# Kernel optimization log

Measured on AMD Instinct MI355X. Metric: run time of the kernel, lower is better.

Reference implementation:

```python
import jax, jax.numpy as jnp
import numpy as np

N_NODES = 100000

def gcn_conv(x, src, dst, dinv, W, b):
    # PyG GCNConv: out[i] = sum_{j->i} dinv[j]*dinv[i] * (x @ W)[j] + b
    h = x @ W                                   # [N, Cout]
    norm = (dinv[src] * dinv[dst])[:, None]     # [E, 1]
    msg = h[src] * norm                         # edge-wise gather + scale
    agg = jax.ops.segment_sum(msg, dst, num_segments=N_NODES)
    return agg + b

def setup_inputs() -> dict:
    key = jax.random.key(0)
    ks = jax.random.split(key, 8)
    x = jax.random.normal(ks[0], (N_NODES, 128), dtype=jnp.float32)
    edge_index = jax.random.randint(ks[1], (2, 1600000), 0, N_NODES, dtype=jnp.int64)
    s = 0.05
    W1 = jax.random.normal(ks[2], (128, 256), dtype=jnp.float32) * s
    b1 = jnp.zeros((256,), dtype=jnp.float32)
    W2 = jax.random.normal(ks[3], (256, 128), dtype=jnp.float32) * s
    b2 = jnp.zeros((128,), dtype=jnp.float32)
    W3 = jax.random.normal(ks[4], (128, 64), dtype=jnp.float32) * s
    b3 = jnp.zeros((64,), dtype=jnp.float32)
    return {"x": x, "edge_index": edge_index, "W1": W1, "b1": b1,
            "W2": W2, "b2": b2, "W3": W3, "b3": b3}

def reference(x, edge_index, W1, b1, W2, b2, W3, b3):
    # add self-loops once (same graph for all three convs)
    loops = jnp.arange(N_NODES, dtype=edge_index.dtype)
    src = jnp.concatenate([edge_index[0], loops])
    dst = jnp.concatenate([edge_index[1], loops])
    # symmetric degree normalization (deg computed on destination, with self-loops)
    deg = jax.ops.segment_sum(jnp.ones_like(dst, dtype=x.dtype), dst, num_segments=N_NODES)
    dinv = jnp.where(deg > 0, jax.lax.rsqrt(jnp.maximum(deg, 1.0)), 0.0)
    h = jax.nn.relu(gcn_conv(x, src, dst, dinv, W1, b1))   # dropout = identity (eval)
    h = jax.nn.relu(gcn_conv(h, src, dst, dinv, W2, b2))
    h = jax.nn.relu(gcn_conv(h, src, dst, dinv, W3, b3))
    return jax.nn.log_softmax(h, axis=1)
```

## Files before the change

### kernel.cpp

```cpp
#include <hip/hip_runtime.h>
#include <math.h>

#define N_NODES 100000
#define N_EDGES 1600000
#define CHUNK 4096
#define NBLK_P ((N_EDGES + CHUNK - 1) / CHUNK)
#define NPAD 100064
#define BSHIFT 8
#define NBUCK ((N_NODES + 255) / 256)
#define BCAP 6144

typedef __attribute__((ext_vector_type(8))) short bf16x8;
typedef __attribute__((ext_vector_type(4))) float f32x4;
typedef __attribute__((ext_vector_type(2))) float f32x2;

__device__ __forceinline__ unsigned short f2bf(float f) {
    unsigned int u = __builtin_bit_cast(unsigned int, f);
    u += 0x7fffu + ((u >> 16) & 1u);
    return (unsigned short)(u >> 16);
}
__device__ __forceinline__ unsigned char f2fp8(float f) {
    return (unsigned char)(__builtin_amdgcn_cvt_pk_fp8_f32(f, f, 0, false) & 0xff);
}
__device__ __forceinline__ f32x2 fp8x2f(unsigned short u) {
    return __builtin_amdgcn_cvt_pk_f32_fp8((int)u, false);
}
__device__ __forceinline__ float fp8f(unsigned char u) {
    return __builtin_amdgcn_cvt_f32_fp8((int)u, 0);
}


__global__ __launch_bounds__(1024) void edge_count_kernel(const int* __restrict__ dst,
                                                          int* __restrict__ bcnt) {
    __shared__ int lh[NBUCK];
    int tid = threadIdx.x;
    if (tid < NBUCK) lh[tid] = 0;
    __syncthreads();
    long base = (long)blockIdx.x * CHUNK;
#pragma unroll
    for (int p = 0; p < CHUNK; p += 1024) {
        long e = base + p + tid;
        if (e < N_EDGES) atomicAdd(&lh[dst[e] >> BSHIFT], 1);
    }
    __syncthreads();
    if (tid < NBUCK) bcnt[tid * NBLK_P + blockIdx.x] = lh[tid];
}


__global__ void bucket_scan_kernel(int* __restrict__ bcnt, int* __restrict__ btot) {
    int bu = blockIdx.x, lane = threadIdx.x;
    int base = 0;
    for (int i0 = 0; i0 < NBLK_P; i0 += 64) {
        int i = i0 + lane;
        int v = (i < NBLK_P) ? bcnt[bu * NBLK_P + i] : 0;
        int orig = v;
#pragma unroll
        for (int off = 1; off < 64; off <<= 1) {
            int t = __shfl_up(v, off);
            if (lane >= off) v += t;
        }
        if (i < NBLK_P) bcnt[bu * NBLK_P + i] = base + v - orig;
        base += __shfl(v, 63);
    }
    if (lane == 0) btot[bu] = base;
}

__global__ void bbase_scan_kernel(const int* __restrict__ btot, int* __restrict__ bbase) {
    __shared__ int tmp[512];
    int i = threadIdx.x;
    int v = (i < NBUCK) ? btot[i] : 0;
    tmp[i] = v;
    __syncthreads();
    for (int off = 1; off < 512; off <<= 1) {
        int t = (i >= off) ? tmp[i - off] : 0;
        __syncthreads();
        tmp[i] += t;
        __syncthreads();
    }
    if (i < NBUCK) bbase[i] = tmp[i] - v;
}


__global__ __launch_bounds__(1024) void part_scatter_kernel(
        const int* __restrict__ src, const int* __restrict__ dst,
        const int* __restrict__ bcnt, const int* __restrict__ bbase,
        int* __restrict__ part) {
    __shared__ int lh[NBUCK];
    int tid = threadIdx.x;
    if (tid < NBUCK) lh[tid] = 0;
    __syncthreads();
    long base = (long)blockIdx.x * CHUNK;
#pragma unroll
    for (int p = 0; p < CHUNK; p += 1024) {
        long e = base + p + tid;
        if (e < N_EDGES) {
            int s = src[e], d = dst[e];
            int bu = d >> BSHIFT;
            int lr = atomicAdd(&lh[bu], 1);
            int pos = bbase[bu] + bcnt[bu * NBLK_P + blockIdx.x] + lr;
            part[pos] = s | ((d & 255) << 17);
        }
    }
}


__global__ __launch_bounds__(512) void bucket_deg_kernel(
        const int* __restrict__ part, const int* __restrict__ bbase,
        const int* __restrict__ btot, int* __restrict__ rowp,
        float* __restrict__ dinv) {
    __shared__ int lcnt[256];
    __shared__ int lscan[256];
    int b = blockIdx.x;
    int node0 = b << BSHIFT;
    int start = bbase[b];
    int cnt = btot[b];
    int tid = threadIdx.x;
    if (tid < 256) lcnt[tid] = 0;
    __syncthreads();
    for (int e = tid; e < cnt; e += 512)
        atomicAdd(&lcnt[part[start + e] >> 17], 1);
    __syncthreads();
    int v = 0;
    if (tid < 256) { v = lcnt[tid]; lscan[tid] = v; }
    __syncthreads();
    for (int off = 1; off < 256; off <<= 1) {
        int t = (tid < 256 && tid >= off) ? lscan[tid - off] : 0;
        __syncthreads();
        if (tid < 256) lscan[tid] += t;
        __syncthreads();
    }
    if (tid < 256) {
        int n = node0 + tid;
        if (n < N_NODES) {
            rowp[n] = start + lscan[tid] - v;
            dinv[n] = rsqrtf(1.0f + (float)v);
        }
    }
    if (b == NBUCK - 1 && tid == 0) rowp[N_NODES] = N_EDGES;
}


__global__ __launch_bounds__(512) void final_scatter_lds_kernel(
        const int* __restrict__ part, const float* __restrict__ dinv,
        const int* __restrict__ rowp, const int* __restrict__ bbase,
        const int* __restrict__ btot, int2* __restrict__ sedge) {
    __shared__ int lcurs[256];
    __shared__ int2 buf[BCAP];
    int b = blockIdx.x;
    int node0 = b << BSHIFT;
    int start = bbase[b];
    int cnt = btot[b];
    int tid = threadIdx.x;
    if (tid < 256) {
        int n = node0 + tid;
        lcurs[tid] = (n < N_NODES) ? (rowp[n] - start) : cnt;
    }
    __syncthreads();
    for (int e = tid; e < cnt; e += 512) {
        int r = part[start + e];
        int s = r & 0x1FFFF;
        int lpos = atomicAdd(&lcurs[r >> 17], 1);
        int2 rec; rec.x = s; rec.y = __float_as_int(dinv[s]);
        if (lpos < BCAP) buf[lpos] = rec;
        else sedge[start + lpos] = rec;
    }
    __syncthreads();
    int lim = min(cnt, BCAP);
    for (int e = tid; e < lim; e += 512)
        sedge[start + e] = buf[e];
}


__global__ void cvt_x_kernel(const float* __restrict__ x, unsigned char* __restrict__ xb) {
    long i = (long)blockIdx.x * blockDim.x + threadIdx.x;
    if (i >= (long)N_NODES * 128 / 4) return;
    float4 v = ((const float4*)x)[i];
    int p0 = __builtin_amdgcn_cvt_pk_fp8_f32(v.x, v.y, 0, false);
    int p1 = __builtin_amdgcn_cvt_pk_fp8_f32(v.z, v.w, 0, false);
    ((unsigned int*)xb)[i] = ((unsigned int)p0 & 0xffffu) | ((unsigned int)p1 << 16);
}

__global__ void cvt_w_all_kernel(const float* __restrict__ W1, const float* __restrict__ W2,
                                 const float* __restrict__ W3,
                                 unsigned short* __restrict__ Wt1,
                                 unsigned short* __restrict__ Wt2,
                                 unsigned short* __restrict__ Wt3) {
    int i = blockIdx.x * blockDim.x + threadIdx.x;
    if (i < 32768) {
        int k = i >> 8, m = i & 255;
        Wt1[m * 128 + k] = f2bf(W1[i]);
    } else if (i < 65536) {
        int j = i - 32768;
        int k = j >> 7, m = j & 127;
        Wt2[m * 256 + k] = f2bf(W2[j]);
    } else if (i < 73728) {
        int j = i - 65536;
        int k = j >> 6, m = j & 63;
        Wt3[m * 128 + k] = f2bf(W3[j]);
    }
}


template<int C, bool BIAS, bool RELU, bool LOGSM, bool OUTF32>
__global__ __launch_bounds__(64) void agg_csr_kernel(
                               const unsigned char* __restrict__ h8,
                               const float* __restrict__ dinv,
                               const int* __restrict__ rowptr,
                               const int2* __restrict__ sedge,
                               const float* __restrict__ bias, void* __restrict__ outv) {
    constexpr int V = C / 64;
    int gw = blockIdx.x;
    int lane = threadIdx.x;
    if (gw >= N_NODES) return;

    float di = dinv[gw];
    int st = rowptr[gw];
    int cnt = rowptr[gw + 1] - st;
    float a0, a1 = 0.0f;
    if constexpr (V == 2) {
        unsigned short u = ((const unsigned short*)(h8 + (long)gw * C))[lane];
        f32x2 f = fp8x2f(u);
        a0 = di * f.x; a1 = di * f.y;
    } else {
        a0 = di * fp8f(h8[(long)gw * C + lane]);
    }

    int k = 0;
    for (; k + 8 <= cnt; k += 8) {
        int2 r[8];
#pragma unroll
        for (int j = 0; j < 8; ++j) r[j] = sedge[st + k + j];
        if constexpr (V == 2) {
            unsigned short u[8];
#pragma unroll
            for (int j = 0; j < 8; ++j)
                u[j] = ((const unsigned short*)(h8 + (long)r[j].x * C))[lane];
#pragma unroll
            for (int j = 0; j < 8; ++j) {
                float w = __int_as_float(r[j].y);
                f32x2 f = fp8x2f(u[j]);
                a0 += w * f.x; a1 += w * f.y;
            }
        } else {
            unsigned char u[8];
#pragma unroll
            for (int j = 0; j < 8; ++j)
                u[j] = h8[(long)r[j].x * C + lane];
#pragma unroll
            for (int j = 0; j < 8; ++j)
                a0 += __int_as_float(r[j].y) * fp8f(u[j]);
        }
    }
    for (; k + 4 <= cnt; k += 4) {
        int2 r[4];
#pragma unroll
        for (int j = 0; j < 4; ++j) r[j] = sedge[st + k + j];
        if constexpr (V == 2) {
            unsigned short u[4];
#pragma unroll
            for (int j = 0; j < 4; ++j)
                u[j] = ((const unsigned short*)(h8 + (long)r[j].x * C))[lane];
#pragma unroll
            for (int j = 0; j < 4; ++j) {
                float w = __int_as_float(r[j].y);
                f32x2 f = fp8x2f(u[j]);
                a0 += w * f.x; a1 += w * f.y;
            }
        } else {
            unsigned char u[4];
#pragma unroll
            for (int j = 0; j < 4; ++j)
                u[j] = h8[(long)r[j].x * C + lane];
#pragma unroll
            for (int j = 0; j < 4; ++j)
                a0 += __int_as_float(r[j].y) * fp8f(u[j]);
        }
    }
    for (; k < cnt; ++k) {
        int2 r = sedge[st + k];
        float w = __int_as_float(r.y);
        if constexpr (V == 2) {
            unsigned short u = ((const unsigned short*)(h8 + (long)r.x * C))[lane];
            f32x2 f = fp8x2f(u);
            a0 += w * f.x; a1 += w * f.y;
        } else {
            a0 += w * fp8f(h8[(long)r.x * C + lane]);
        }
    }

    a0 *= di; a1 *= di;
    if constexpr (BIAS) {
        if constexpr (V == 2) { a0 += bias[lane * 2]; a1 += bias[lane * 2 + 1]; }
        else a0 += bias[lane];
    }
    if constexpr (RELU) { a0 = fmaxf(a0, 0.0f); a1 = fmaxf(a1, 0.0f); }
    if constexpr (LOGSM) {
        float m = a0;
#pragma unroll
        for (int o = 32; o > 0; o >>= 1) m = fmaxf(m, __shfl_xor(m, o));
        float e = expf(a0 - m), s = e;
#pragma unroll
        for (int o = 32; o > 0; o >>= 1) s += __shfl_xor(s, o);
        a0 = a0 - m - logf(s);
    }
    if constexpr (OUTF32) {
        float* out = (float*)outv;
        if constexpr (V == 2) {
            float2 r; r.x = a0; r.y = a1;
            *(float2*)(out + (long)gw * C + lane * 2) = r;
        } else {
            out[(long)gw * C + lane] = a0;
        }
    } else {
        unsigned short* out = (unsigned short*)outv;
        if constexpr (V == 2) {
            unsigned int up = (unsigned int)f2bf(a0) | ((unsigned int)f2bf(a1) << 16);
            ((unsigned int*)(out + (long)gw * C))[lane] = up;
        } else {
            out[(long)gw * C + lane] = f2bf(a0);
        }
    }
}

template<int K, int M, bool BIAS, bool RELU, bool OUT8>
__global__ __launch_bounds__(256) void gemm_mfma_kernel(
        const unsigned short* __restrict__ A,
        const unsigned short* __restrict__ Bt,
        const float* __restrict__ bias,
        void* __restrict__ Cv,
        int N) {
    constexpr int KC = K / 8;
    constexpr int NT = M / 64;
    __shared__ unsigned short As[64 * K];

    int tid = threadIdx.x;
    int row0 = blockIdx.x * 64;
    const unsigned short* Ap = A + (long)row0 * K;

    for (int c = tid; c < 64 * KC; c += 256) {
        int r = c / KC;
        unsigned int swz = ((unsigned int)c * 16u) ^ ((unsigned int)(r & 7) << 4);
        *(bf16x8*)((char*)As + swz) = *(const bf16x8*)(Ap + c * 8);
    }
    __syncthreads();

    int lane = tid & 63;
    int wv = tid >> 6;
    int lr = lane & 15;
    int kg = lane >> 4;
    int colbase = wv * (M / 4);

    const unsigned short* bp[NT];
#pragma unroll
    for (int ni = 0; ni < NT; ++ni)
        bp[ni] = Bt + (size_t)(colbase + ni * 16 + lr) * K + kg * 8;

    f32x4 acc[4][NT] = {};

    for (int k0 = 0; k0 < K; k0 += 32) {
        bf16x8 a[4], b[NT];
#pragma unroll
        for (int mi = 0; mi < 4; ++mi) {
            int r = mi * 16 + lr;
            unsigned int byteo = (unsigned int)((r * K + k0 + kg * 8) * 2);
            byteo ^= (unsigned int)((r & 7) << 4);
            a[mi] = *(const bf16x8*)((const char*)As + byteo);
        }
#pragma unroll
        for (int ni = 0; ni < NT; ++ni)
            b[ni] = *(const bf16x8*)(bp[ni] + k0);
#pragma unroll
        for (int mi = 0; mi < 4; ++mi)
#pragma unroll
            for (int ni = 0; ni < NT; ++ni)
                acc[mi][ni] = __builtin_amdgcn_mfma_f32_16x16x32_bf16(
                    a[mi], b[ni], acc[mi][ni], 0, 0, 0);
    }

#pragma unroll
    for (int mi = 0; mi < 4; ++mi) {
#pragma unroll
        for (int ni = 0; ni < NT; ++ni) {
            int col = colbase + ni * 16 + lr;
            float bv = BIAS ? bias[col] : 0.0f;
#pragma unroll
            for (int i = 0; i < 4; ++i) {
                int row = row0 + mi * 16 + kg * 4 + i;
                if (row < N) {
                    float v = acc[mi][ni][i] + bv;
                    if (RELU) v = fmaxf(v, 0.0f);
                    if constexpr (OUT8)
                        ((unsigned char*)Cv)[(long)row * M + col] = f2fp8(v);
                    else
                        ((unsigned short*)Cv)[(long)row * M + col] = f2bf(v);
                }
            }
        }
    }
}


extern "C" void kernel_launch(void* const* d_in, const int* in_sizes, int n_in,
                              void* d_out, int out_size, void* d_ws, size_t ws_size,
                              hipStream_t stream) {
    const float* x  = (const float*)d_in[0];
    const int* edge = (const int*)d_in[1];
    const float* W1 = (const float*)d_in[2];
    const float* b1 = (const float*)d_in[3];
    const float* W2 = (const float*)d_in[4];
    const float* b2 = (const float*)d_in[5];
    const float* W3 = (const float*)d_in[6];
    const float* b3 = (const float*)d_in[7];
    float* out = (float*)d_out;

    const int* src = edge;
    const int* dst = edge + N_EDGES;

    float* ws    = (float*)d_ws;
    float* dinv  = ws;
    int*   rowp  = (int*)(ws + 100000);
    int*   btot  = (int*)(ws + 200352);
    int*   bbase = (int*)(ws + 200864);
    int*   bcnt  = (int*)(ws + 201376);
    int2*  sedge = (int2*)(ws + 354976);
    unsigned char*  X8 = (unsigned char*)(ws + 3554976);
    unsigned short* B1 = (unsigned short*)(ws + 6757024);
    unsigned short* B2 = (unsigned short*)(ws + 13161120);
    unsigned char*  Q2 = (unsigned char*)(ws + 25969312);
    unsigned short* Wt1 = (unsigned short*)(ws + 29171360);
    unsigned short* Wt2 = Wt1 + 128 * 256;
    unsigned short* Wt3 = Wt2 + 256 * 128;
    int*   part  = (int*)B2;

    const int BT = 256;
    int gRows = (N_NODES + 63) / 64;

    edge_count_kernel<<<NBLK_P, 1024, 0, stream>>>(dst, bcnt);

    bucket_scan_kernel<<<NBUCK, 64, 0, stream>>>(bcnt, btot);
    bbase_scan_kernel<<<1, 512, 0, stream>>>(btot, bbase);
    part_scatter_kernel<<<NBLK_P, 1024, 0, stream>>>(src, dst, bcnt, bbase, part);

    bucket_deg_kernel<<<NBUCK, 512, 0, stream>>>(part, bbase, btot, rowp, dinv);
    final_scatter_lds_kernel<<<NBUCK, 512, 0, stream>>>(part, dinv, rowp, bbase, btot, sedge);

    cvt_x_kernel<<<(int)(((long)N_NODES * 128 / 4 + BT - 1) / BT), BT, 0, stream>>>(x, X8);
    cvt_w_all_kernel<<<(73728 + BT - 1) / BT, BT, 0, stream>>>(W1, W2, W3, Wt1, Wt2, Wt3);

    agg_csr_kernel<128, false, false, false, false><<<N_NODES, 64, 0, stream>>>(
        X8, dinv, rowp, sedge, nullptr, B1);
    gemm_mfma_kernel<128, 256, true, true, false><<<gRows, BT, 0, stream>>>(
        B1, Wt1, b1, B2, N_NODES);

    gemm_mfma_kernel<256, 128, false, false, true><<<gRows, BT, 0, stream>>>(
        B2, Wt2, nullptr, Q2, N_NODES);
    agg_csr_kernel<128, true, true, false, false><<<N_NODES, 64, 0, stream>>>(
        Q2, dinv, rowp, sedge, b2, B1);

    gemm_mfma_kernel<128, 64, false, false, true><<<gRows, BT, 0, stream>>>(
        B1, Wt3, nullptr, Q2, N_NODES);
    agg_csr_kernel<64, true, true, true, true><<<N_NODES, 64, 0, stream>>>(
        Q2, dinv, rowp, sedge, b3, out);

    (void)in_sizes; (void)n_in; (void)out_size; (void)ws_size;
}
```

Baseline: 275.6 us.

## Pack CSR edge records into 32 bits with quantized weights; merge conversion kernels

Each sorted edge record shrinks from an int2 (source index plus float dinv) to one 32-bit word: a 17-bit source index and a 15-bit fixed-point dinv. The three aggregation passes decode it with a mask, shift and multiply. This halves the edge-stream bytes read in every aggregation and in the scatter's LDS buffer, at the cost of quantizing the normalization weight. The x and weight conversion kernels are also merged into one launch to save a launch.

```diff
diff --git a/kernel.cpp b/kernel.cpp
--- a/kernel.cpp
+++ b/kernel.cpp
@@ -27,6 +27,9 @@
 }
 __device__ __forceinline__ float fp8f(unsigned char u) {
     return __builtin_amdgcn_cvt_f32_fp8((int)u, 0);
+}
+__device__ __forceinline__ float decw(unsigned int r) {
+    return (float)(r >> 17) * (1.0f / 32767.0f);
 }
 
 
@@ -143,9 +146,9 @@
 __global__ __launch_bounds__(512) void final_scatter_lds_kernel(
         const int* __restrict__ part, const float* __restrict__ dinv,
         const int* __restrict__ rowp, const int* __restrict__ bbase,
-        const int* __restrict__ btot, int2* __restrict__ sedge) {
+        const int* __restrict__ btot, unsigned int* __restrict__ sedge) {
     __shared__ int lcurs[256];
-    __shared__ int2 buf[BCAP];
+    __shared__ unsigned int buf[BCAP];
     int b = blockIdx.x;
     int node0 = b << BSHIFT;
     int start = bbase[b];
@@ -160,7 +163,8 @@
         int r = part[start + e];
         int s = r & 0x1FFFF;
         int lpos = atomicAdd(&lcurs[r >> 17], 1);
-        int2 rec; rec.x = s; rec.y = __float_as_int(dinv[s]);
+        unsigned int q = (unsigned int)(dinv[s] * 32767.0f + 0.5f);
+        unsigned int rec = (unsigned int)s | (q << 17);
         if (lpos < BCAP) buf[lpos] = rec;
         else sedge[start + lpos] = rec;
     }
@@ -171,32 +175,34 @@
 }
 
 
-__global__ void cvt_x_kernel(const float* __restrict__ x, unsigned char* __restrict__ xb) {
+#define CVT_X_ITEMS 3200000
+
+__global__ void cvt_all_kernel(const float* __restrict__ x, unsigned char* __restrict__ xb,
+                               const float* __restrict__ W1, const float* __restrict__ W2,
+                               const float* __restrict__ W3,
+                               unsigned short* __restrict__ Wt1,
+                               unsigned short* __restrict__ Wt2,
+                               unsigned short* __restrict__ Wt3) {
     long i = (long)blockIdx.x * blockDim.x + threadIdx.x;
-    if (i >= (long)N_NODES * 128 / 4) return;
-    float4 v = ((const float4*)x)[i];
-    int p0 = __builtin_amdgcn_cvt_pk_fp8_f32(v.x, v.y, 0, false);
-    int p1 = __builtin_amdgcn_cvt_pk_fp8_f32(v.z, v.w, 0, false);
-    ((unsigned int*)xb)[i] = ((unsigned int)p0 & 0xffffu) | ((unsigned int)p1 << 16);
-}
-
-__global__ void cvt_w_all_kernel(const float* __restrict__ W1, const float* __restrict__ W2,
-                                 const float* __restrict__ W3,
-                                 unsigned short* __restrict__ Wt1,
-                                 unsigned short* __restrict__ Wt2,
-                                 unsigned short* __restrict__ Wt3) {
-    int i = blockIdx.x * blockDim.x + threadIdx.x;
-    if (i < 32768) {
-        int k = i >> 8, m = i & 255;
-        Wt1[m * 128 + k] = f2bf(W1[i]);
-    } else if (i < 65536) {
-        int j = i - 32768;
-        int k = j >> 7, m = j & 127;
-        Wt2[m * 256 + k] = f2bf(W2[j]);
-    } else if (i < 73728) {
-        int j = i - 65536;
-        int k = j >> 6, m = j & 63;
-        Wt3[m * 128 + k] = f2bf(W3[j]);
+    if (i < CVT_X_ITEMS) {
+        float4 v = ((const float4*)x)[i];
+        int p0 = __builtin_amdgcn_cvt_pk_fp8_f32(v.x, v.y, 0, false);
+        int p1 = __builtin_amdgcn_cvt_pk_fp8_f32(v.z, v.w, 0, false);
+        ((unsigned int*)xb)[i] = ((unsigned int)p0 & 0xffffu) | ((unsigned int)p1 << 16);
+        return;
+    }
+    int j = (int)(i - CVT_X_ITEMS);
+    if (j < 32768) {
+        int k = j >> 8, m = j & 255;
+        Wt1[m * 128 + k] = f2bf(W1[j]);
+    } else if (j < 65536) {
+        int t = j - 32768;
+        int k = t >> 7, m = t & 127;
+        Wt2[m * 256 + k] = f2bf(W2[t]);
+    } else if (j < 73728) {
+        int t = j - 65536;
+        int k = t >> 6, m = t & 63;
+        Wt3[m * 128 + k] = f2bf(W3[t]);
     }
 }
 
@@ -206,7 +212,7 @@
                                const unsigned char* __restrict__ h8,
                                const float* __restrict__ dinv,
                                const int* __restrict__ rowptr,
-                               const int2* __restrict__ sedge,
+                               const unsigned int* __restrict__ sedge,
                                const float* __restrict__ bias, void* __restrict__ outv) {
     constexpr int V = C / 64;
     int gw = blockIdx.x;
@@ -227,17 +233,17 @@
 
     int k = 0;
     for (; k + 8 <= cnt; k += 8) {
-        int2 r[8];
+        unsigned int r[8];
 #pragma unroll
         for (int j = 0; j < 8; ++j) r[j] = sedge[st + k + j];
         if constexpr (V == 2) {
             unsigned short u[8];
 #pragma unroll
             for (int j = 0; j < 8; ++j)
-                u[j] = ((const unsigned short*)(h8 + (long)r[j].x * C))[lane];
+                u[j] = ((const unsigned short*)(h8 + (long)(r[j] & 0x1FFFF) * C))[lane];
 #pragma unroll
             for (int j = 0; j < 8; ++j) {
-                float w = __int_as_float(r[j].y);
+                float w = decw(r[j]);
                 f32x2 f = fp8x2f(u[j]);
                 a0 += w * f.x; a1 += w * f.y;
             }
@@ -245,24 +251,24 @@
             unsigned char u[8];
 #pragma unroll
             for (int j = 0; j < 8; ++j)
-                u[j] = h8[(long)r[j].x * C + lane];
+                u[j] = h8[(long)(r[j] & 0x1FFFF) * C + lane];
 #pragma unroll
             for (int j = 0; j < 8; ++j)
-                a0 += __int_as_float(r[j].y) * fp8f(u[j]);
+                a0 += decw(r[j]) * fp8f(u[j]);
         }
     }
     for (; k + 4 <= cnt; k += 4) {
-        int2 r[4];
+        unsigned int r[4];
 #pragma unroll
         for (int j = 0; j < 4; ++j) r[j] = sedge[st + k + j];
         if constexpr (V == 2) {
             unsigned short u[4];
 #pragma unroll
             for (int j = 0; j < 4; ++j)
-                u[j] = ((const unsigned short*)(h8 + (long)r[j].x * C))[lane];
+                u[j] = ((const unsigned short*)(h8 + (long)(r[j] & 0x1FFFF) * C))[lane];
 #pragma unroll
             for (int j = 0; j < 4; ++j) {
-                float w = __int_as_float(r[j].y);
+                float w = decw(r[j]);
                 f32x2 f = fp8x2f(u[j]);
                 a0 += w * f.x; a1 += w * f.y;
             }
@@ -270,21 +276,21 @@
             unsigned char u[4];
 #pragma unroll
             for (int j = 0; j < 4; ++j)
-                u[j] = h8[(long)r[j].x * C + lane];
+                u[j] = h8[(long)(r[j] & 0x1FFFF) * C + lane];
 #pragma unroll
             for (int j = 0; j < 4; ++j)
-                a0 += __int_as_float(r[j].y) * fp8f(u[j]);
+                a0 += decw(r[j]) * fp8f(u[j]);
         }
     }
     for (; k < cnt; ++k) {
-        int2 r = sedge[st + k];
-        float w = __int_as_float(r.y);
+        unsigned int r = sedge[st + k];
+        float w = decw(r);
         if constexpr (V == 2) {
-            unsigned short u = ((const unsigned short*)(h8 + (long)r.x * C))[lane];
+            unsigned short u = ((const unsigned short*)(h8 + (long)(r & 0x1FFFF) * C))[lane];
             f32x2 f = fp8x2f(u);
             a0 += w * f.x; a1 += w * f.y;
         } else {
-            a0 += w * fp8f(h8[(long)r.x * C + lane]);
+            a0 += w * fp8f(h8[(long)(r & 0x1FFFF) * C + lane]);
         }
     }
 
@@ -422,12 +428,12 @@
     int*   btot  = (int*)(ws + 200352);
     int*   bbase = (int*)(ws + 200864);
     int*   bcnt  = (int*)(ws + 201376);
-    int2*  sedge = (int2*)(ws + 354976);
-    unsigned char*  X8 = (unsigned char*)(ws + 3554976);
-    unsigned short* B1 = (unsigned short*)(ws + 6757024);
-    unsigned short* B2 = (unsigned short*)(ws + 13161120);
-    unsigned char*  Q2 = (unsigned char*)(ws + 25969312);
-    unsigned short* Wt1 = (unsigned short*)(ws + 29171360);
+    unsigned int* sedge = (unsigned int*)(ws + 354976);
+    unsigned char*  X8 = (unsigned char*)(ws + 1954976);
+    unsigned short* B1 = (unsigned short*)(ws + 5157024);
+    unsigned short* B2 = (unsigned short*)(ws + 11561120);
+    unsigned char*  Q2 = (unsigned char*)(ws + 24369312);
+    unsigned short* Wt1 = (unsigned short*)(ws + 27571360);
     unsigned short* Wt2 = Wt1 + 128 * 256;
     unsigned short* Wt3 = Wt2 + 256 * 128;
     int*   part  = (int*)B2;
@@ -444,8 +450,8 @@
     bucket_deg_kernel<<<NBUCK, 512, 0, stream>>>(part, bbase, btot, rowp, dinv);
     final_scatter_lds_kernel<<<NBUCK, 512, 0, stream>>>(part, dinv, rowp, bbase, btot, sedge);
 
-    cvt_x_kernel<<<(int)(((long)N_NODES * 128 / 4 + BT - 1) / BT), BT, 0, stream>>>(x, X8);
-    cvt_w_all_kernel<<<(73728 + BT - 1) / BT, BT, 0, stream>>>(W1, W2, W3, Wt1, Wt2, Wt3);
+    cvt_all_kernel<<<(int)((CVT_X_ITEMS + 73728 + BT - 1) / BT), BT, 0, stream>>>(
+        x, X8, W1, W2, W3, Wt1, Wt2, Wt3);
 
     agg_csr_kernel<128, false, false, false, false><<<N_NODES, 64, 0, stream>>>(
         X8, dinv, rowp, sedge, nullptr, B1);
```

After: 264.4 us, median of 2. -4.1%, faster.
